# Performance work log

Hardware: AMD Instinct MI355X
Metric: run time of the kernel (lower is better)

The kernel has to match this reference:

```python
import jax, jax.numpy as jnp
import numpy as np

PR = np.float32(0.7)
RA = np.float32(1e6)
LAM_DATA = 1.0
LAM_TB = 1.0
LAM_CONTI = 1.0
LAM_NSE = 1.0
LAM_EE = 1.0


def _act(a):
    return 0.5 * jnp.sin(2.0 * jnp.pi * a)


def _mlp(x, W_in, b_in, W_hid, b_hid, W_out, b_out):
    # x: (..., 4) -> (..., 4); 6 hidden layers of width D, sin activation
    h = _act(x @ W_in + b_in)
    for i in range(W_hid.shape[0]):  # static small loop over hidden layers
        h = _act(h @ W_hid[i] + b_hid[i])
    return h @ W_out + b_out


def setup_inputs() -> dict:
    key = jax.random.key(0)
    ks = jax.random.split(key, 6)
    N, D = 4096, 128
    inputs = jax.random.uniform(ks[0], (N, 4), dtype=jnp.float32)
    y_true = jax.random.normal(ks[1], (N, 4), dtype=jnp.float32)
    W_in = jax.random.normal(ks[2], (4, D), dtype=jnp.float32) / jnp.sqrt(4.0)
    b_in = jnp.zeros((D,), jnp.float32)
    W_hid = jax.random.normal(ks[3], (5, D, D), dtype=jnp.float32) / jnp.sqrt(float(D))
    b_hid = jnp.zeros((5, D), jnp.float32)
    W_out = jax.random.normal(ks[4], (D, 4), dtype=jnp.float32) / jnp.sqrt(float(D))
    b_out = jnp.zeros((4,), jnp.float32)
    return {"inputs": inputs, "y_true": y_true, "W_in": W_in, "b_in": b_in,
            "W_hid": W_hid, "b_hid": b_hid, "W_out": W_out, "b_out": b_out}


def reference(inputs, y_true, W_in, b_in, W_hid, b_hid, W_out, b_out):
    # input order: (t, x, y, z) = indices (0,1,2,3); output order: (u, v, w, T)
    f = lambda xi: _mlp(xi, W_in, b_in, W_hid, b_hid, W_out, b_out)  # R^4 -> R^4
    y_pred = _mlp(inputs, W_in, b_in, W_hid, b_hid, W_out, b_out)    # (N,4)
    # Per-point derivative tensors via nested forward-mode (replaces ~30 tape.gradient calls)
    J = jax.vmap(jax.jacfwd(f))(inputs)                               # (N, out, d1)
    H = jax.vmap(jax.jacfwd(jax.jacfwd(f)))(inputs)                   # (N, out, d1, d2)
    G3 = jax.vmap(jax.jacfwd(jax.jacfwd(jax.jacfwd(f))))(inputs)      # (N, out, d1, d2, d3)

    u, v, w = y_pred[:, 0], y_pred[:, 1], y_pred[:, 2]
    u_x, u_y, u_z = J[:, 0, 1], J[:, 0, 2], J[:, 0, 3]
    v_x, v_y, v_z = J[:, 1, 1], J[:, 1, 2], J[:, 1, 3]
    w_x, w_y, w_z = J[:, 2, 1], J[:, 2, 2], J[:, 2, 3]
    T_t, T_x, T_y, T_z = J[:, 3, 0], J[:, 3, 1], J[:, 3, 2], J[:, 3, 3]

    s = jnp.sqrt(PR / RA)
    kappa = np.float32(np.sqrt(1.0 / (0.7 * 1e6)))

    # data loss: MSE over (u,v,w)
    loss_data = jnp.mean(jnp.square(y_pred[:, :3] - y_true[:, :3]))

    # temperature boundary loss at z in {0,1}
    N = inputs.shape[0]
    kb1, kb2 = jax.random.split(jax.random.key(22))
    xy_b = jax.random.uniform(kb1, (N, 2), dtype=inputs.dtype)
    z_b = jax.random.randint(kb2, (N, 1), 0, 2).astype(inputs.dtype)
    inp_b = jnp.concatenate([inputs[:, :1], xy_b, z_b], axis=1)
    T_b = _mlp(inp_b, W_in, b_in, W_hid, b_hid, W_out, b_out)[:, 3]
    T_true_b = jnp.where(z_b[:, 0] == 0.0, 0.5, -0.5)  # T_max at z=0, T_min at z=1
    loss_Tb = jnp.mean(jnp.square(T_true_b - T_b))

    # continuity
    loss_conti = jnp.mean(jnp.square(u_x + v_y + w_z))

    # vorticity-form NSE residuals
    NSE_u = (H[:, 2, 2, 0] - H[:, 1, 3, 0]
             + u * (H[:, 2, 2, 1] - H[:, 1, 3, 1])
             + v * (H[:, 2, 2, 2] - H[:, 1, 3, 2])
             + w * (H[:, 2, 2, 3] - H[:, 1, 3, 3])
             - (w_y - v_z) * u_x - (u_z - w_x) * u_y - (v_x - u_y) * u_z
             - s * (G3[:, 2, 2, 1, 1] - G3[:, 1, 3, 1, 1]
                    + G3[:, 2, 2, 2, 2] - G3[:, 1, 3, 2, 2]
                    + G3[:, 2, 2, 3, 3] - G3[:, 1, 3, 3, 3])
             - T_y)
    NSE_v = (H[:, 0, 3, 0] - H[:, 2, 1, 0]
             + u * (H[:, 0, 3, 1] - H[:, 2, 1, 1])
             + v * (H[:, 0, 3, 2] - H[:, 2, 1, 2])
             + w * (H[:, 0, 3, 3] - H[:, 2, 1, 3])
             - (w_y - v_z) * v_x - (u_z - w_x) * v_y - (v_x - u_y) * v_z
             - s * (G3[:, 0, 3, 1, 1] - G3[:, 2, 1, 1, 1]
                    + G3[:, 0, 3, 2, 2] - G3[:, 2, 1, 2, 2]
                    + G3[:, 0, 3, 3, 3] - G3[:, 2, 1, 3, 3])
             + T_x)
    NSE_w = (H[:, 1, 1, 0] - H[:, 0, 2, 0]
             + u * (H[:, 1, 1, 1] - H[:, 0, 2, 1])
             + v * (H[:, 1, 1, 2] - H[:, 0, 2, 2])
             + w * (H[:, 1, 1, 3] - H[:, 0, 2, 3])
             - (w_y - v_z) * w_x - (u_z - w_x) * w_y - (v_x - u_y) * w_z
             - s * (G3[:, 1, 1, 1, 1] - G3[:, 0, 2, 1, 1]
                    + G3[:, 1, 1, 2, 2] - G3[:, 0, 2, 2, 2]
                    + G3[:, 1, 1, 3, 3] - G3[:, 0, 2, 3, 3]))
    loss_NSE = jnp.mean(jnp.square(jnp.stack([NSE_u, NSE_v, NSE_w])))

    # energy equation
    EE = T_t + u * T_x + v * T_y + w * T_z - kappa * (H[:, 3, 1, 1] + H[:, 3, 2, 2] + H[:, 3, 3, 3])
    loss_EE = jnp.mean(jnp.square(EE))

    total = (LAM_DATA * loss_data + LAM_CONTI * loss_conti + LAM_NSE * loss_NSE
             + LAM_EE * loss_EE + LAM_TB * loss_Tb)
    return total
```

## Files before the change

### kernel.cpp

```cpp
#include <hip/hip_runtime.h>
#include <math.h>

#define NPTS 4096
#define DD   128
#define NCH  24
#define NHID 5
#define PPB  4
#define BS   256
#define WP8  17
#define WPW  68
#define PLSZ 26112
#define OSM_OFF 52224
#define ROWM(p,c) (16*((c)>>2) + 4*(p) + ((c)&3))

typedef __attribute__((ext_vector_type(8))) _Float16 half8;
typedef __attribute__((ext_vector_type(2))) __fp16 fp16x2;
typedef __attribute__((ext_vector_type(4))) float f32x4;

#define SS_INV 1024.0f
#define ST_INV 65536.0f

static __device__ __forceinline__ unsigned short f2h_bits(float x) {
  _Float16 h = (_Float16)x; unsigned short u; __builtin_memcpy(&u, &h, 2); return u;
}
static __device__ __forceinline__ unsigned pk2(float a, float b) {
  fp16x2 h = __builtin_amdgcn_cvt_pkrtz(a, b);
  unsigned u; __builtin_memcpy(&u, &h, 4); return u;
}

static __device__ __forceinline__ void tf2x32(unsigned k0, unsigned k1,
                                              unsigned x0, unsigned x1,
                                              unsigned &o0, unsigned &o1) {
  unsigned ks2 = 0x1BD11BDAu ^ k0 ^ k1;
  x0 += k0; x1 += k1;
#define TFR(r) { x0 += x1; x1 = (x1 << (r)) | (x1 >> (32 - (r))); x1 ^= x0; }
  TFR(13) TFR(15) TFR(26) TFR(6)  x0 += k1;  x1 += ks2 + 1u;
  TFR(17) TFR(29) TFR(16) TFR(24) x0 += ks2; x1 += k0 + 2u;
  TFR(13) TFR(15) TFR(26) TFR(6)  x0 += k0;  x1 += k1 + 3u;
  TFR(17) TFR(29) TFR(16) TFR(24) x0 += k1;  x1 += ks2 + 4u;
  TFR(13) TFR(15) TFR(26) TFR(6)  x0 += ks2; x1 += k0 + 5u;
#undef TFR
  o0 = x0; o1 = x1;
}
static __device__ __forceinline__ float bits_to_unif(unsigned b) {
  return __uint_as_float((b >> 9) | 0x3f800000u) - 1.0f;
}
static __device__ __forceinline__ void bnd_rand(int pt, float &xb1, float &xb2,
                                                unsigned &zbit) {
  unsigned a0, a1, b0, b1;
  tf2x32(0u, 22u, 0u, 2u, a0, b0);
  tf2x32(0u, 22u, 1u, 3u, a1, b1);
  unsigned f0, f1, zf, o0_, o1_;
  unsigned jj0 = 2u * (unsigned)pt, jj1 = jj0 + 1u;
  if (jj0 < 4096u) { tf2x32(a0, a1, jj0,         jj0 + 4096u, o0_, o1_); f0 = o0_; }
  else             { tf2x32(a0, a1, jj0 - 4096u, jj0,         o0_, o1_); f0 = o1_; }
  if (jj1 < 4096u) { tf2x32(a0, a1, jj1,         jj1 + 4096u, o0_, o1_); f1 = o0_; }
  else             { tf2x32(a0, a1, jj1 - 4096u, jj1,         o0_, o1_); f1 = o1_; }
  if (pt < 2048)   { tf2x32(b0, b1, (unsigned)pt,         (unsigned)pt + 2048u, o0_, o1_); zf = o0_; }
  else             { tf2x32(b0, b1, (unsigned)pt - 2048u, (unsigned)pt,         o0_, o1_); zf = o1_; }
  xb1 = bits_to_unif(f0); xb2 = bits_to_unif(f1); zbit = zf & 1u;
}

static __device__ __forceinline__ void activate_jet(float q[NCH]) {
  const float PI1 = 3.14159265358979323846f;
  float hr = q[0] - floorf(q[0]);
  float sv = __builtin_amdgcn_sinf(hr);
  float cv = __builtin_amdgcn_cosf(hr);
  float p1 = PI1 * cv;
  float p2  = -2.0f * PI1 * PI1 * sv;
  float p3  = -4.0f * PI1 * PI1 * PI1 * cv;
  float p2s = p2 * 9.765625e-4f;
  float p2t = p2 * 0.015625f;
  float p3t = p3 * 1.52587890625e-5f;
  float g0 = q[1], g1 = q[2], g2 = q[3], g3 = q[4];
  float s_tx = q[5], s_ty = q[6], s_tz = q[7], s_xx = q[8], s_xy = q[9],
        s_xz = q[10], s_yy = q[11], s_yz = q[12], s_zz = q[13];
  float T0 = q[14], T1 = q[15], T2 = q[16], T3 = q[17], T4 = q[18],
        T5 = q[19], T6 = q[20], T7 = q[21], T8 = q[22];
  q[0] = 0.5f * sv;
  q[1] = p1 * g0; q[2] = p1 * g1; q[3] = p1 * g2; q[4] = p1 * g3;
  q[5]  = p2s * g0 * g1 + p1 * s_tx;
  q[6]  = p2s * g0 * g2 + p1 * s_ty;
  q[7]  = p2s * g0 * g3 + p1 * s_tz;
  q[8]  = p2s * g1 * g1 + p1 * s_xx;
  q[9]  = p2s * g1 * g2 + p1 * s_xy;
  q[10] = p2s * g1 * g3 + p1 * s_xz;
  q[11] = p2s * g2 * g2 + p1 * s_yy;
  q[12] = p2s * g2 * g3 + p1 * s_yz;
  q[13] = p2s * g3 * g3 + p1 * s_zz;
  q[14] = p3t * g1 * g1 * g1 + p2t * (3.0f * s_xx * g1)              + p1 * T0;
  q[15] = p3t * g2 * g1 * g1 + p2t * (2.0f * s_xy * g1 + s_xx * g2)  + p1 * T1;
  q[16] = p3t * g3 * g1 * g1 + p2t * (2.0f * s_xz * g1 + s_xx * g3)  + p1 * T2;
  q[17] = p3t * g1 * g2 * g2 + p2t * (2.0f * s_xy * g2 + s_yy * g1)  + p1 * T3;
  q[18] = p3t * g2 * g2 * g2 + p2t * (3.0f * s_yy * g2)              + p1 * T4;
  q[19] = p3t * g3 * g2 * g2 + p2t * (2.0f * s_yz * g2 + s_yy * g3)  + p1 * T5;
  q[20] = p3t * g1 * g3 * g3 + p2t * (2.0f * s_xz * g3 + s_zz * g1)  + p1 * T6;
  q[21] = p3t * g2 * g3 * g3 + p2t * (2.0f * s_yz * g3 + s_zz * g2)  + p1 * T7;
  q[22] = p3t * g3 * g3 * g3 + p2t * (3.0f * s_zz * g3)              + p1 * T8;
  float br = q[23] - floorf(q[23]);
  q[23] = 0.5f * __builtin_amdgcn_sinf(br);
}

__global__ __launch_bounds__(256) void prep_kernel(
    const float* __restrict__ W_hid, const float* __restrict__ W_out,
    unsigned short* __restrict__ wsh, unsigned short* __restrict__ aoh,
    float4* __restrict__ rnd, float* __restrict__ out) {
  int b = blockIdx.x;
  if (b == 0 && threadIdx.x == 0) out[0] = 0.0f;
  if (b < 320) {
    int idx = b * 256 + threadIdx.x;
    int l = idx >> 14, r = idx & 16383;
    int nt = r >> 11, r2 = r & 2047;
    int ks = r2 >> 9, r3 = r2 & 511;
    int nl = r3 >> 5, r4 = r3 & 31;
    int quad = r4 >> 3, e = r4 & 7;
    int jin  = 32 * ks + 16 * (e & 1) + 4 * quad + (e >> 1);
    int jout = nt * 16 + nl;
    wsh[idx] = f2h_bits(W_hid[(l << 14) + (jin << 7) + jout]);
  } else if (b < 328) {
    int idx = (b - 320) * 256 + threadIdx.x;
    int ks = idx >> 9, r3 = idx & 511;
    int nl = r3 >> 5, r4 = r3 & 31;
    int quad = r4 >> 3, e = r4 & 7;
    int jin = 32 * ks + 16 * (e & 1) + 4 * quad + (e >> 1);
    aoh[idx] = f2h_bits((nl < 4) ? W_out[jin * 4 + nl] : 0.0f);
  } else {
    int pt = (b - 328) * 256 + threadIdx.x;
    float xb1, xb2; unsigned zbit;
    bnd_rand(pt, xb1, xb2, zbit);
    rnd[pt] = make_float4(xb1, xb2, (float)zbit, zbit ? -0.5f : 0.5f);
  }
}

__global__ __launch_bounds__(BS, 3) void pinn_kernel(
    const float* __restrict__ inputs, const float* __restrict__ y_true,
    const float* __restrict__ W_in,  const float* __restrict__ b_in,
    const float* __restrict__ b_hid, const float* __restrict__ b_out,
    const unsigned short* __restrict__ wsh,
    const unsigned short* __restrict__ aoh,
    const float4* __restrict__ rnd,
    float* __restrict__ out)
{
  __shared__ __align__(16) unsigned char smem[53760];
  _Float16* plane0 = (_Float16*)smem;
  _Float16* plane1 = (_Float16*)(smem + PLSZ);
  float* Osm = (float*)(smem + OSM_OFF);

  const int t    = threadIdx.x;
  const int wave = t >> 6;
  const int lane = t & 63;
  const int q    = lane >> 4;
  const int nl   = lane & 15;
  const int P    = 16 * wave + nl;
  const int ja   = 32 * wave + nl;
  const int jb   = ja + 16;
  const int pt0  = blockIdx.x * PPB;

  const half8* wh8 = (const half8*)wsh;
  const half8* oh8 = (const half8*)aoh;

  half8 wr[2][8];
#pragma unroll
  for (int z = 0; z < 8; ++z) {
    int i = z >> 2, ks = z & 3;
    wr[0][z] = wh8[((2 * wave + i) * 4 + ks) * 64 + nl * 4 + q];
  }

  {
    const int p1 = t >> 6;
    const int P1 = lane;
    const int j1a = 32 * (P1 >> 4) + (P1 & 15), j1b = j1a + 16;
    const int pt = pt0 + p1;
    float4 rv = rnd[pt];
    float x_t = inputs[pt * 4 + 0], x_x = inputs[pt * 4 + 1];
    float x_y = inputs[pt * 4 + 2], x_z = inputs[pt * 4 + 3];
    float q0[NCH], q1[NCH];
#pragma unroll
    for (int h = 0; h < 2; ++h) {
      int jj = h ? j1b : j1a;
      float* qq = h ? q1 : q0;
      float w0 = W_in[0 * DD + jj], w1 = W_in[1 * DD + jj],
            w2 = W_in[2 * DD + jj], w3 = W_in[3 * DD + jj];
      float bb = b_in[jj];
      qq[0] = bb + x_t * w0 + x_x * w1 + x_y * w2 + x_z * w3;
      qq[1] = w0; qq[2] = w1; qq[3] = w2; qq[4] = w3;
#pragma unroll
      for (int c = 5; c < 23; ++c) qq[c] = 0.0f;
      qq[23] = bb + x_t * w0 + rv.x * w1 + rv.y * w2 + rv.z * w3;
      activate_jet(qq);
    }
    unsigned* dw = (unsigned*)plane0;
#pragma unroll
    for (int c = 0; c < NCH; ++c)
      dw[ROWM(p1, c) * WPW + P1] = pk2(q0[c], q1[c]);
  }
  __syncthreads();

#pragma unroll
  for (int l = 0; l < NHID; ++l) {
    const half8* src = (const half8*)((l & 1) ? plane1 : plane0);
    unsigned* dstw = (unsigned*)((l & 1) ? plane0 : plane1);

    f32x4 acc[6][2];
#pragma unroll
    for (int mt = 0; mt < 6; ++mt) { acc[mt][0] = (f32x4)0.0f; acc[mt][1] = (f32x4)0.0f; }

#pragma unroll
    for (int ks = 0; ks < 4; ++ks) {
      half8 a[6];
#pragma unroll
      for (int mt = 0; mt < 6; ++mt)
        a[mt] = src[(16 * mt + nl) * WP8 + ks * 4 + q];
#pragma unroll
      for (int mt = 0; mt < 6; ++mt)
#pragma unroll
        for (int i = 0; i < 2; ++i)
          acc[mt][i] = __builtin_amdgcn_mfma_f32_16x16x32_f16(a[mt], wr[l & 1][i * 4 + ks], acc[mt][i], 0, 0, 0);
    }

    if (l + 1 < NHID) {
#pragma unroll
      for (int z = 0; z < 8; ++z) {
        int i = z >> 2, ks = z & 3;
        wr[(l + 1) & 1][z] = wh8[(((l + 1) * 8 + 2 * wave + i) * 4 + ks) * 64 + nl * 4 + q];
      }
    }

    float qa[NCH], qb[NCH];
#pragma unroll
    for (int mt = 0; mt < 6; ++mt)
#pragma unroll
      for (int r = 0; r < 4; ++r) {
        qa[4 * mt + r] = acc[mt][0][r];
        qb[4 * mt + r] = acc[mt][1][r];
      }
    float ba = b_hid[l * DD + ja], bb_ = b_hid[l * DD + jb];
    qa[0] += ba; qa[23] += ba;
    qb[0] += bb_; qb[23] += bb_;
    activate_jet(qa);
    activate_jet(qb);
#pragma unroll
    for (int c = 0; c < NCH; ++c)
      dstw[ROWM(q, c) * WPW + P] = pk2(qa[c], qb[c]);
    __syncthreads();
  }

  {
    const half8* src = (const half8*)plane1;
    if (wave < 3) {
      f32x4 acc2[2];
      acc2[0] = (f32x4)0.0f; acc2[1] = (f32x4)0.0f;
#pragma unroll
      for (int ks = 0; ks < 4; ++ks) {
        half8 a0 = src[(16 * (2 * wave)     + nl) * WP8 + ks * 4 + q];
        half8 a1 = src[(16 * (2 * wave + 1) + nl) * WP8 + ks * 4 + q];
        half8 oh = oh8[ks * 64 + nl * 4 + q];
        acc2[0] = __builtin_amdgcn_mfma_f32_16x16x32_f16(a0, oh, acc2[0], 0, 0, 0);
        acc2[1] = __builtin_amdgcn_mfma_f32_16x16x32_f16(a1, oh, acc2[1], 0, 0, 0);
      }
      if (nl < 4) {
#pragma unroll
        for (int i = 0; i < 2; ++i)
#pragma unroll
          for (int r = 0; r < 4; ++r)
            Osm[(q * NCH + 4 * (2 * wave + i) + r) * 4 + nl] = acc2[i][r];
      }
    }
  }
  __syncthreads();

  if (t < PPB) {
    const int pp = t;
    const int ptt = pt0 + pp;
    const float Ttrue = rnd[ptt].w;
    const float SEC  = SS_INV;
    const float SCT  = 8.36660026534e-04f * ST_INV;
    const float KAPS = 1.19522860933e-03f * SS_INV;
    float bo0 = b_out[0], bo1 = b_out[1], bo2 = b_out[2], bo3 = b_out[3];
#define OO(o, c) Osm[(pp * NCH + (c)) * 4 + (o)]
    float u  = OO(0, 0) + bo0, v_ = OO(1, 0) + bo1, w_ = OO(2, 0) + bo2;
    float ux = OO(0, 2), uy = OO(0, 3), uz = OO(0, 4);
    float vx = OO(1, 2), vy = OO(1, 3), vz = OO(1, 4);
    float wx = OO(2, 2), wy = OO(2, 3), wz = OO(2, 4);
    float Tt = OO(3, 1), Tx = OO(3, 2), Ty = OO(3, 3), Tz = OO(3, 4);

    float hu = OO(2, 6) - OO(1, 7)
             + u  * (OO(2, 9)  - OO(1, 10))
             + v_ * (OO(2, 11) - OO(1, 12))
             + w_ * (OO(2, 12) - OO(1, 13));
    float NSEu = SEC * hu
               - (wy - vz) * ux - (uz - wx) * uy - (vx - uy) * uz
               - SCT * (OO(2, 15) - OO(1, 16) + OO(2, 18) - OO(1, 19) + OO(2, 21) - OO(1, 22))
               - Ty;
    float hv = OO(0, 7) - OO(2, 5)
             + u  * (OO(0, 10) - OO(2, 8))
             + v_ * (OO(0, 12) - OO(2, 9))
             + w_ * (OO(0, 13) - OO(2, 10));
    float NSEv = SEC * hv
               - (wy - vz) * vx - (uz - wx) * vy - (vx - uy) * vz
               - SCT * (OO(0, 16) - OO(2, 14) + OO(0, 19) - OO(2, 17) + OO(0, 22) - OO(2, 20))
               + Tx;
    float hw = OO(1, 5) - OO(0, 6)
             + u  * (OO(1, 8)  - OO(0, 9))
             + v_ * (OO(1, 9)  - OO(0, 11))
             + w_ * (OO(1, 10) - OO(0, 12));
    float NSEw = SEC * hw
               - (wy - vz) * wx - (uz - wx) * wy - (vx - uy) * wz
               - SCT * (OO(1, 14) - OO(0, 15) + OO(1, 17) - OO(0, 18) + OO(1, 20) - OO(0, 21));

    float EE = Tt + u * Tx + v_ * Ty + w_ * Tz
             - KAPS * (OO(3, 8) + OO(3, 11) + OO(3, 13));

    float conti = ux + vy + wz;
    const float* yt = y_true + ptt * 4;
    float d0 = u - yt[0], d1 = v_ - yt[1], d2 = w_ - yt[2];
    float dT = Ttrue - (OO(3, 23) + bo3);
#undef OO
    const float invN  = 1.0f / (float)NPTS;
    const float inv3N = 1.0f / (3.0f * (float)NPTS);
    float part = (d0 * d0 + d1 * d1 + d2 * d2) * inv3N
               + conti * conti * invN
               + (NSEu * NSEu + NSEv * NSEv + NSEw * NSEw) * inv3N
               + EE * EE * invN
               + dT * dT * invN;
    atomicAdd(out, part);
  }
}

extern "C" void kernel_launch(void* const* d_in, const int* in_sizes, int n_in,
                              void* d_out, int out_size, void* d_ws, size_t ws_size,
                              hipStream_t stream) {
  const float* inputs = (const float*)d_in[0];
  const float* y_true = (const float*)d_in[1];
  const float* W_in   = (const float*)d_in[2];
  const float* b_in   = (const float*)d_in[3];
  const float* W_hid  = (const float*)d_in[4];
  const float* b_hid  = (const float*)d_in[5];
  const float* W_out  = (const float*)d_in[6];
  const float* b_out  = (const float*)d_in[7];
  float* out = (float*)d_out;

  unsigned char* ws = (unsigned char*)d_ws;
  unsigned short* wsh = (unsigned short*)(ws);
  unsigned short* aoh = (unsigned short*)(ws + 163840);
  float4*         rnd = (float4*)(ws + 167936);

  prep_kernel<<<344, 256, 0, stream>>>(W_hid, W_out, wsh, aoh, rnd, out);
  pinn_kernel<<<NPTS / PPB, BS, 0, stream>>>(inputs, y_true, W_in, b_in,
                                             b_hid, b_out, wsh, aoh, rnd, out);
}
```

Before: 95.65 us.

## Single-buffer activation plane and compute boundary random inline

Replaces the two ping-pong LDS activation planes with one plane, reading and writing it in place with an extra barrier between the MFMA reads and the activation writes. This roughly halves LDS per block, so more blocks can be resident per CU. It also drops the precomputed random-boundary buffer and recomputes the hash in the main kernel, removing a global load and a small slice of the prep kernel. The costs are an extra sync per layer, a loop that is no longer forced to unroll, and repeated hash arithmetic.

```diff
diff --git a/kernel.cpp b/kernel.cpp
--- a/kernel.cpp
+++ b/kernel.cpp
@@ -10,7 +10,7 @@
 #define WP8  17
 #define WPW  68
 #define PLSZ 26112
-#define OSM_OFF 52224
+#define OSM_OFF 26112
 #define ROWM(p,c) (16*((c)>>2) + 4*(p) + ((c)&3))
 
 typedef __attribute__((ext_vector_type(8))) _Float16 half8;
@@ -104,7 +104,7 @@
 __global__ __launch_bounds__(256) void prep_kernel(
     const float* __restrict__ W_hid, const float* __restrict__ W_out,
     unsigned short* __restrict__ wsh, unsigned short* __restrict__ aoh,
-    float4* __restrict__ rnd, float* __restrict__ out) {
+    float* __restrict__ out) {
   int b = blockIdx.x;
   if (b == 0 && threadIdx.x == 0) out[0] = 0.0f;
   if (b < 320) {
@@ -117,18 +117,13 @@
     int jin  = 32 * ks + 16 * (e & 1) + 4 * quad + (e >> 1);
     int jout = nt * 16 + nl;
     wsh[idx] = f2h_bits(W_hid[(l << 14) + (jin << 7) + jout]);
-  } else if (b < 328) {
+  } else {
     int idx = (b - 320) * 256 + threadIdx.x;
     int ks = idx >> 9, r3 = idx & 511;
     int nl = r3 >> 5, r4 = r3 & 31;
     int quad = r4 >> 3, e = r4 & 7;
     int jin = 32 * ks + 16 * (e & 1) + 4 * quad + (e >> 1);
     aoh[idx] = f2h_bits((nl < 4) ? W_out[jin * 4 + nl] : 0.0f);
-  } else {
-    int pt = (b - 328) * 256 + threadIdx.x;
-    float xb1, xb2; unsigned zbit;
-    bnd_rand(pt, xb1, xb2, zbit);
-    rnd[pt] = make_float4(xb1, xb2, (float)zbit, zbit ? -0.5f : 0.5f);
   }
 }
 
@@ -138,12 +133,10 @@
     const float* __restrict__ b_hid, const float* __restrict__ b_out,
     const unsigned short* __restrict__ wsh,
     const unsigned short* __restrict__ aoh,
-    const float4* __restrict__ rnd,
     float* __restrict__ out)
 {
-  __shared__ __align__(16) unsigned char smem[53760];
-  _Float16* plane0 = (_Float16*)smem;
-  _Float16* plane1 = (_Float16*)(smem + PLSZ);
+  __shared__ __align__(16) unsigned char smem[27648];
+  _Float16* plane = (_Float16*)smem;
   float* Osm = (float*)(smem + OSM_OFF);
 
   const int t    = threadIdx.x;
@@ -171,9 +164,11 @@
     const int P1 = lane;
     const int j1a = 32 * (P1 >> 4) + (P1 & 15), j1b = j1a + 16;
     const int pt = pt0 + p1;
-    float4 rv = rnd[pt];
+    float xb1, xb2; unsigned zbit;
+    bnd_rand(pt, xb1, xb2, zbit);
     float x_t = inputs[pt * 4 + 0], x_x = inputs[pt * 4 + 1];
     float x_y = inputs[pt * 4 + 2], x_z = inputs[pt * 4 + 3];
+    float zbf = (float)zbit;
     float q0[NCH], q1[NCH];
 #pragma unroll
     for (int h = 0; h < 2; ++h) {
@@ -186,20 +181,19 @@
       qq[1] = w0; qq[2] = w1; qq[3] = w2; qq[4] = w3;
 #pragma unroll
       for (int c = 5; c < 23; ++c) qq[c] = 0.0f;
-      qq[23] = bb + x_t * w0 + rv.x * w1 + rv.y * w2 + rv.z * w3;
+      qq[23] = bb + x_t * w0 + xb1 * w1 + xb2 * w2 + zbf * w3;
       activate_jet(qq);
     }
-    unsigned* dw = (unsigned*)plane0;
+    unsigned* dw = (unsigned*)plane;
 #pragma unroll
     for (int c = 0; c < NCH; ++c)
       dw[ROWM(p1, c) * WPW + P1] = pk2(q0[c], q1[c]);
   }
   __syncthreads();
 
-#pragma unroll
   for (int l = 0; l < NHID; ++l) {
-    const half8* src = (const half8*)((l & 1) ? plane1 : plane0);
-    unsigned* dstw = (unsigned*)((l & 1) ? plane0 : plane1);
+    const half8* src = (const half8*)plane;
+    unsigned* dstw = (unsigned*)plane;
 
     f32x4 acc[6][2];
 #pragma unroll
@@ -225,6 +219,7 @@
         wr[(l + 1) & 1][z] = wh8[(((l + 1) * 8 + 2 * wave + i) * 4 + ks) * 64 + nl * 4 + q];
       }
     }
+    __syncthreads();
 
     float qa[NCH], qb[NCH];
 #pragma unroll
@@ -246,7 +241,7 @@
   }
 
   {
-    const half8* src = (const half8*)plane1;
+    const half8* src = (const half8*)plane;
     if (wave < 3) {
       f32x4 acc2[2];
       acc2[0] = (f32x4)0.0f; acc2[1] = (f32x4)0.0f;
@@ -272,7 +267,9 @@
   if (t < PPB) {
     const int pp = t;
     const int ptt = pt0 + pp;
-    const float Ttrue = rnd[ptt].w;
+    float xb1_, xb2_; unsigned zbit;
+    bnd_rand(ptt, xb1_, xb2_, zbit);
+    const float Ttrue = zbit ? -0.5f : 0.5f;
     const float SEC  = SS_INV;
     const float SCT  = 8.36660026534e-04f * ST_INV;
     const float KAPS = 1.19522860933e-03f * SS_INV;
@@ -343,9 +340,8 @@
   unsigned char* ws = (unsigned char*)d_ws;
   unsigned short* wsh = (unsigned short*)(ws);
   unsigned short* aoh = (unsigned short*)(ws + 163840);
-  float4*         rnd = (float4*)(ws + 167936);
-
-  prep_kernel<<<344, 256, 0, stream>>>(W_hid, W_out, wsh, aoh, rnd, out);
+
+  prep_kernel<<<328, 256, 0, stream>>>(W_hid, W_out, wsh, aoh, out);
   pinn_kernel<<<NPTS / PPB, BS, 0, stream>>>(inputs, y_true, W_in, b_in,
-                                             b_hid, b_out, wsh, aoh, rnd, out);
-}
+                                             b_hid, b_out, wsh, aoh, out);
+}
```

Result: slower. 98.87 us (+3.4%).

## Double block size to 512 threads, one output column tile per wave

Applied to the files above, without the earlier changes.

Raises the block from 4 to 8 waves. Each wave now owns one 16-column output tile per hidden layer instead of two, so each wave holds half as many weight fragments and accumulators. The jet activation per thread is halved and the writes to shared memory become 16-bit scattered stores with an interleaved slot mapping instead of packed pairs. Launch bounds now ask for 4 blocks per CU to raise occupancy, at the cost of more threads per barrier and narrower, possibly bank-conflicting LDS stores.

```diff
diff --git a/kernel.cpp b/kernel.cpp
--- a/kernel.cpp
+++ b/kernel.cpp
@@ -6,15 +6,14 @@
 #define NCH  24
 #define NHID 5
 #define PPB  4
-#define BS   256
+#define BS   512
 #define WP8  17
-#define WPW  68
+#define WPU  136
 #define PLSZ 26112
 #define OSM_OFF 52224
 #define ROWM(p,c) (16*((c)>>2) + 4*(p) + ((c)&3))
 
 typedef __attribute__((ext_vector_type(8))) _Float16 half8;
-typedef __attribute__((ext_vector_type(2))) __fp16 fp16x2;
 typedef __attribute__((ext_vector_type(4))) float f32x4;
 
 #define SS_INV 1024.0f
@@ -22,10 +21,6 @@
 
 static __device__ __forceinline__ unsigned short f2h_bits(float x) {
   _Float16 h = (_Float16)x; unsigned short u; __builtin_memcpy(&u, &h, 2); return u;
-}
-static __device__ __forceinline__ unsigned pk2(float a, float b) {
-  fp16x2 h = __builtin_amdgcn_cvt_pkrtz(a, b);
-  unsigned u; __builtin_memcpy(&u, &h, 4); return u;
 }
 
 static __device__ __forceinline__ void tf2x32(unsigned k0, unsigned k1,
@@ -132,7 +127,7 @@
   }
 }
 
-__global__ __launch_bounds__(BS, 3) void pinn_kernel(
+__global__ __launch_bounds__(BS, 4) void pinn_kernel(
     const float* __restrict__ inputs, const float* __restrict__ y_true,
     const float* __restrict__ W_in,  const float* __restrict__ b_in,
     const float* __restrict__ b_hid, const float* __restrict__ b_out,
@@ -151,59 +146,51 @@
   const int lane = t & 63;
   const int q    = lane >> 4;
   const int nl   = lane & 15;
-  const int P    = 16 * wave + nl;
-  const int ja   = 32 * wave + nl;
-  const int jb   = ja + 16;
+  const int j    = 16 * wave + nl;
+  const int slt  = 32 * (wave >> 1) + 2 * nl + (wave & 1);
   const int pt0  = blockIdx.x * PPB;
 
   const half8* wh8 = (const half8*)wsh;
   const half8* oh8 = (const half8*)aoh;
 
-  half8 wr[2][8];
-#pragma unroll
-  for (int z = 0; z < 8; ++z) {
-    int i = z >> 2, ks = z & 3;
-    wr[0][z] = wh8[((2 * wave + i) * 4 + ks) * 64 + nl * 4 + q];
-  }
+  half8 wr[2][4];
+#pragma unroll
+  for (int ks = 0; ks < 4; ++ks)
+    wr[0][ks] = wh8[(wave * 4 + ks) * 64 + nl * 4 + q];
 
   {
-    const int p1 = t >> 6;
-    const int P1 = lane;
-    const int j1a = 32 * (P1 >> 4) + (P1 & 15), j1b = j1a + 16;
+    const int p1 = t >> 7;
+    const int j1 = t & 127;
+    const int s1 = 32 * (j1 >> 5) + 2 * (j1 & 15) + ((j1 >> 4) & 1);
     const int pt = pt0 + p1;
     float4 rv = rnd[pt];
     float x_t = inputs[pt * 4 + 0], x_x = inputs[pt * 4 + 1];
     float x_y = inputs[pt * 4 + 2], x_z = inputs[pt * 4 + 3];
-    float q0[NCH], q1[NCH];
-#pragma unroll
-    for (int h = 0; h < 2; ++h) {
-      int jj = h ? j1b : j1a;
-      float* qq = h ? q1 : q0;
-      float w0 = W_in[0 * DD + jj], w1 = W_in[1 * DD + jj],
-            w2 = W_in[2 * DD + jj], w3 = W_in[3 * DD + jj];
-      float bb = b_in[jj];
-      qq[0] = bb + x_t * w0 + x_x * w1 + x_y * w2 + x_z * w3;
-      qq[1] = w0; qq[2] = w1; qq[3] = w2; qq[4] = w3;
-#pragma unroll
-      for (int c = 5; c < 23; ++c) qq[c] = 0.0f;
-      qq[23] = bb + x_t * w0 + rv.x * w1 + rv.y * w2 + rv.z * w3;
-      activate_jet(qq);
-    }
-    unsigned* dw = (unsigned*)plane0;
+    float qq[NCH];
+    float w0 = W_in[0 * DD + j1], w1 = W_in[1 * DD + j1],
+          w2 = W_in[2 * DD + j1], w3 = W_in[3 * DD + j1];
+    float bb = b_in[j1];
+    qq[0] = bb + x_t * w0 + x_x * w1 + x_y * w2 + x_z * w3;
+    qq[1] = w0; qq[2] = w1; qq[3] = w2; qq[4] = w3;
+#pragma unroll
+    for (int c = 5; c < 23; ++c) qq[c] = 0.0f;
+    qq[23] = bb + x_t * w0 + rv.x * w1 + rv.y * w2 + rv.z * w3;
+    activate_jet(qq);
+    unsigned short* d16 = (unsigned short*)plane0;
 #pragma unroll
     for (int c = 0; c < NCH; ++c)
-      dw[ROWM(p1, c) * WPW + P1] = pk2(q0[c], q1[c]);
+      d16[ROWM(p1, c) * WPU + s1] = f2h_bits(qq[c]);
   }
   __syncthreads();
 
 #pragma unroll
   for (int l = 0; l < NHID; ++l) {
     const half8* src = (const half8*)((l & 1) ? plane1 : plane0);
-    unsigned* dstw = (unsigned*)((l & 1) ? plane0 : plane1);
-
-    f32x4 acc[6][2];
-#pragma unroll
-    for (int mt = 0; mt < 6; ++mt) { acc[mt][0] = (f32x4)0.0f; acc[mt][1] = (f32x4)0.0f; }
+    unsigned short* d16 = (unsigned short*)((l & 1) ? plane0 : plane1);
+
+    f32x4 acc[6];
+#pragma unroll
+    for (int mt = 0; mt < 6; ++mt) acc[mt] = (f32x4)0.0f;
 
 #pragma unroll
     for (int ks = 0; ks < 4; ++ks) {
@@ -213,57 +200,44 @@
         a[mt] = src[(16 * mt + nl) * WP8 + ks * 4 + q];
 #pragma unroll
       for (int mt = 0; mt < 6; ++mt)
-#pragma unroll
-        for (int i = 0; i < 2; ++i)
-          acc[mt][i] = __builtin_amdgcn_mfma_f32_16x16x32_f16(a[mt], wr[l & 1][i * 4 + ks], acc[mt][i], 0, 0, 0);
+        acc[mt] = __builtin_amdgcn_mfma_f32_16x16x32_f16(a[mt], wr[l & 1][ks], acc[mt], 0, 0, 0);
     }
 
     if (l + 1 < NHID) {
 #pragma unroll
-      for (int z = 0; z < 8; ++z) {
-        int i = z >> 2, ks = z & 3;
-        wr[(l + 1) & 1][z] = wh8[(((l + 1) * 8 + 2 * wave + i) * 4 + ks) * 64 + nl * 4 + q];
-      }
+      for (int ks = 0; ks < 4; ++ks)
+        wr[(l + 1) & 1][ks] = wh8[(((l + 1) * 8 + wave) * 4 + ks) * 64 + nl * 4 + q];
     }
 
-    float qa[NCH], qb[NCH];
+    float qq[NCH];
 #pragma unroll
     for (int mt = 0; mt < 6; ++mt)
 #pragma unroll
-      for (int r = 0; r < 4; ++r) {
-        qa[4 * mt + r] = acc[mt][0][r];
-        qb[4 * mt + r] = acc[mt][1][r];
-      }
-    float ba = b_hid[l * DD + ja], bb_ = b_hid[l * DD + jb];
-    qa[0] += ba; qa[23] += ba;
-    qb[0] += bb_; qb[23] += bb_;
-    activate_jet(qa);
-    activate_jet(qb);
+      for (int r = 0; r < 4; ++r)
+        qq[4 * mt + r] = acc[mt][r];
+    float bb = b_hid[l * DD + j];
+    qq[0] += bb; qq[23] += bb;
+    activate_jet(qq);
 #pragma unroll
     for (int c = 0; c < NCH; ++c)
-      dstw[ROWM(q, c) * WPW + P] = pk2(qa[c], qb[c]);
+      d16[ROWM(q, c) * WPU + slt] = f2h_bits(qq[c]);
     __syncthreads();
   }
 
   {
     const half8* src = (const half8*)plane1;
-    if (wave < 3) {
-      f32x4 acc2[2];
-      acc2[0] = (f32x4)0.0f; acc2[1] = (f32x4)0.0f;
+    if (wave < 6) {
+      f32x4 acc2 = (f32x4)0.0f;
 #pragma unroll
       for (int ks = 0; ks < 4; ++ks) {
-        half8 a0 = src[(16 * (2 * wave)     + nl) * WP8 + ks * 4 + q];
-        half8 a1 = src[(16 * (2 * wave + 1) + nl) * WP8 + ks * 4 + q];
+        half8 a0 = src[(16 * wave + nl) * WP8 + ks * 4 + q];
         half8 oh = oh8[ks * 64 + nl * 4 + q];
-        acc2[0] = __builtin_amdgcn_mfma_f32_16x16x32_f16(a0, oh, acc2[0], 0, 0, 0);
-        acc2[1] = __builtin_amdgcn_mfma_f32_16x16x32_f16(a1, oh, acc2[1], 0, 0, 0);
+        acc2 = __builtin_amdgcn_mfma_f32_16x16x32_f16(a0, oh, acc2, 0, 0, 0);
       }
       if (nl < 4) {
 #pragma unroll
-        for (int i = 0; i < 2; ++i)
-#pragma unroll
-          for (int r = 0; r < 4; ++r)
-            Osm[(q * NCH + 4 * (2 * wave + i) + r) * 4 + nl] = acc2[i][r];
+        for (int r = 0; r < 4; ++r)
+          Osm[(q * NCH + 4 * wave + r) * 4 + nl] = acc2[r];
       }
     }
   }
```

Result: no change. 96.05 us (+0.4%).

## Drop prep kernel; load fp32 weights and compute boundary randoms inline

Applied to the files above, without the earlier changes.

Removes the separate prep kernel that pre-converted W_hid/W_out to fp16 in MFMA-friendly layout and precomputed boundary random points. The main kernel now gathers fp32 weights with strided scalar loads, converts them to fp16 in registers, and recomputes the threefry randoms per point, while a memset zeroes the output. This removes one kernel launch and its global traffic, but every one of the 1024 blocks now issues eight uncoalesced 4-byte loads per weight fragment instead of one 16-byte vector load, which adds load latency and register pressure.

```diff
diff --git a/kernel.cpp b/kernel.cpp
--- a/kernel.cpp
+++ b/kernel.cpp
@@ -20,9 +20,6 @@
 #define SS_INV 1024.0f
 #define ST_INV 65536.0f
 
-static __device__ __forceinline__ unsigned short f2h_bits(float x) {
-  _Float16 h = (_Float16)x; unsigned short u; __builtin_memcpy(&u, &h, 2); return u;
-}
 static __device__ __forceinline__ unsigned pk2(float a, float b) {
   fp16x2 h = __builtin_amdgcn_cvt_pkrtz(a, b);
   unsigned u; __builtin_memcpy(&u, &h, 4); return u;
@@ -101,44 +98,21 @@
   q[23] = 0.5f * __builtin_amdgcn_sinf(br);
 }
 
-__global__ __launch_bounds__(256) void prep_kernel(
-    const float* __restrict__ W_hid, const float* __restrict__ W_out,
-    unsigned short* __restrict__ wsh, unsigned short* __restrict__ aoh,
-    float4* __restrict__ rnd, float* __restrict__ out) {
-  int b = blockIdx.x;
-  if (b == 0 && threadIdx.x == 0) out[0] = 0.0f;
-  if (b < 320) {
-    int idx = b * 256 + threadIdx.x;
-    int l = idx >> 14, r = idx & 16383;
-    int nt = r >> 11, r2 = r & 2047;
-    int ks = r2 >> 9, r3 = r2 & 511;
-    int nl = r3 >> 5, r4 = r3 & 31;
-    int quad = r4 >> 3, e = r4 & 7;
-    int jin  = 32 * ks + 16 * (e & 1) + 4 * quad + (e >> 1);
-    int jout = nt * 16 + nl;
-    wsh[idx] = f2h_bits(W_hid[(l << 14) + (jin << 7) + jout]);
-  } else if (b < 328) {
-    int idx = (b - 320) * 256 + threadIdx.x;
-    int ks = idx >> 9, r3 = idx & 511;
-    int nl = r3 >> 5, r4 = r3 & 31;
-    int quad = r4 >> 3, e = r4 & 7;
-    int jin = 32 * ks + 16 * (e & 1) + 4 * quad + (e >> 1);
-    aoh[idx] = f2h_bits((nl < 4) ? W_out[jin * 4 + nl] : 0.0f);
-  } else {
-    int pt = (b - 328) * 256 + threadIdx.x;
-    float xb1, xb2; unsigned zbit;
-    bnd_rand(pt, xb1, xb2, zbit);
-    rnd[pt] = make_float4(xb1, xb2, (float)zbit, zbit ? -0.5f : 0.5f);
-  }
+static __device__ __forceinline__ half8 ldw(const float* __restrict__ W,
+                                            int l, int nt, int ks, int q, int nl) {
+  const float* base = W + (l << 14) + (32 * ks + 4 * q) * DD + nt * 16 + nl;
+  half8 h;
+#pragma unroll
+  for (int e = 0; e < 8; ++e)
+    h[e] = (_Float16)base[((e >> 1) + 16 * (e & 1)) * DD];
+  return h;
 }
 
 __global__ __launch_bounds__(BS, 3) void pinn_kernel(
     const float* __restrict__ inputs, const float* __restrict__ y_true,
     const float* __restrict__ W_in,  const float* __restrict__ b_in,
-    const float* __restrict__ b_hid, const float* __restrict__ b_out,
-    const unsigned short* __restrict__ wsh,
-    const unsigned short* __restrict__ aoh,
-    const float4* __restrict__ rnd,
+    const float* __restrict__ W_hid, const float* __restrict__ b_hid,
+    const float* __restrict__ W_out, const float* __restrict__ b_out,
     float* __restrict__ out)
 {
   __shared__ __align__(16) unsigned char smem[53760];
@@ -156,14 +130,11 @@
   const int jb   = ja + 16;
   const int pt0  = blockIdx.x * PPB;
 
-  const half8* wh8 = (const half8*)wsh;
-  const half8* oh8 = (const half8*)aoh;
-
   half8 wr[2][8];
 #pragma unroll
   for (int z = 0; z < 8; ++z) {
     int i = z >> 2, ks = z & 3;
-    wr[0][z] = wh8[((2 * wave + i) * 4 + ks) * 64 + nl * 4 + q];
+    wr[0][z] = ldw(W_hid, 0, 2 * wave + i, ks, q, nl);
   }
 
   {
@@ -171,9 +142,11 @@
     const int P1 = lane;
     const int j1a = 32 * (P1 >> 4) + (P1 & 15), j1b = j1a + 16;
     const int pt = pt0 + p1;
-    float4 rv = rnd[pt];
+    float xb1, xb2; unsigned zbit;
+    bnd_rand(pt, xb1, xb2, zbit);
     float x_t = inputs[pt * 4 + 0], x_x = inputs[pt * 4 + 1];
     float x_y = inputs[pt * 4 + 2], x_z = inputs[pt * 4 + 3];
+    float zbf = (float)zbit;
     float q0[NCH], q1[NCH];
 #pragma unroll
     for (int h = 0; h < 2; ++h) {
@@ -186,7 +159,7 @@
       qq[1] = w0; qq[2] = w1; qq[3] = w2; qq[4] = w3;
 #pragma unroll
       for (int c = 5; c < 23; ++c) qq[c] = 0.0f;
-      qq[23] = bb + x_t * w0 + rv.x * w1 + rv.y * w2 + rv.z * w3;
+      qq[23] = bb + x_t * w0 + xb1 * w1 + xb2 * w2 + zbf * w3;
       activate_jet(qq);
     }
     unsigned* dw = (unsigned*)plane0;
@@ -222,7 +195,7 @@
 #pragma unroll
       for (int z = 0; z < 8; ++z) {
         int i = z >> 2, ks = z & 3;
-        wr[(l + 1) & 1][z] = wh8[(((l + 1) * 8 + 2 * wave + i) * 4 + ks) * 64 + nl * 4 + q];
+        wr[(l + 1) & 1][z] = ldw(W_hid, l + 1, 2 * wave + i, ks, q, nl);
       }
     }
 
@@ -252,9 +225,14 @@
       acc2[0] = (f32x4)0.0f; acc2[1] = (f32x4)0.0f;
 #pragma unroll
       for (int ks = 0; ks < 4; ++ks) {
+        half8 oh;
+#pragma unroll
+        for (int e = 0; e < 8; ++e) {
+          int jin = 32 * ks + 16 * (e & 1) + 4 * q + (e >> 1);
+          oh[e] = (_Float16)((nl < 4) ? W_out[jin * 4 + nl] : 0.0f);
+        }
         half8 a0 = src[(16 * (2 * wave)     + nl) * WP8 + ks * 4 + q];
         half8 a1 = src[(16 * (2 * wave + 1) + nl) * WP8 + ks * 4 + q];
-        half8 oh = oh8[ks * 64 + nl * 4 + q];
         acc2[0] = __builtin_amdgcn_mfma_f32_16x16x32_f16(a0, oh, acc2[0], 0, 0, 0);
         acc2[1] = __builtin_amdgcn_mfma_f32_16x16x32_f16(a1, oh, acc2[1], 0, 0, 0);
       }
@@ -272,7 +250,9 @@
   if (t < PPB) {
     const int pp = t;
     const int ptt = pt0 + pp;
-    const float Ttrue = rnd[ptt].w;
+    float xb1_, xb2_; unsigned zbit;
+    bnd_rand(ptt, xb1_, xb2_, zbit);
+    const float Ttrue = zbit ? -0.5f : 0.5f;
     const float SEC  = SS_INV;
     const float SCT  = 8.36660026534e-04f * ST_INV;
     const float KAPS = 1.19522860933e-03f * SS_INV;
@@ -340,12 +320,7 @@
   const float* b_out  = (const float*)d_in[7];
   float* out = (float*)d_out;
 
-  unsigned char* ws = (unsigned char*)d_ws;
-  unsigned short* wsh = (unsigned short*)(ws);
-  unsigned short* aoh = (unsigned short*)(ws + 163840);
-  float4*         rnd = (float4*)(ws + 167936);
-
-  prep_kernel<<<344, 256, 0, stream>>>(W_hid, W_out, wsh, aoh, rnd, out);
+  hipMemsetAsync(out, 0, sizeof(float), stream);
   pinn_kernel<<<NPTS / PPB, BS, 0, stream>>>(inputs, y_true, W_in, b_in,
-                                             b_hid, b_out, wsh, aoh, rnd, out);
-}
+                                             W_hid, b_hid, W_out, b_out, out);
+}
```

Result: slower. 112.6 us (+17.7%).
